# Optimization experiments

Hardware: AMD Instinct MI355X
Metric: run time of the kernel (lower is better)

The kernel has to match this reference:

```python
import jax, jax.numpy as jnp
import numpy as np

N_USERS = 50000
N_ITEMS = 50000
N_NODES = N_USERS + N_ITEMS
DIM = 64
NNZ = 3200000
N_LAYERS = 3


def setup_inputs() -> dict:
    key = jax.random.key(0)
    k1, k2, k3, k4, k5 = jax.random.split(key, 5)
    user_emb = 0.1 * jax.random.normal(k1, (N_USERS, DIM), dtype=jnp.float32)
    item_emb = 0.1 * jax.random.normal(k2, (N_ITEMS, DIM), dtype=jnp.float32)
    # COO representation of the symmetric normalized adjacency matrix
    adj_row = jax.random.randint(k3, (NNZ,), 0, N_NODES, dtype=jnp.int32)
    adj_col = jax.random.randint(k4, (NNZ,), 0, N_NODES, dtype=jnp.int32)
    # normalized adjacency values are small positive numbers (d_i^-1/2 d_j^-1/2)
    adj_vals = jax.random.uniform(k5, (NNZ,), dtype=jnp.float32) * 0.05
    return {"user_emb": user_emb, "item_emb": item_emb,
            "adj_vals": adj_vals, "adj_row": adj_row, "adj_col": adj_col}


def reference(user_emb, item_emb, adj_vals, adj_row, adj_col):
    # X0 = concat(user_embedding, item_embedding)  -> [N, D]
    x = jnp.concatenate([user_emb, item_emb], axis=0)

    def spmm(h):
        # sparse A @ h : gather source rows, scale by edge value, scatter-add to dest
        msgs = adj_vals[:, None] * h[adj_col]          # [nnz, D]
        return jax.ops.segment_sum(msgs, adj_row, num_segments=N_NODES)

    # three stacked LightGCN propagation layers (no transforms, no nonlinearity)
    for _ in range(N_LAYERS):
        x = spmm(x)
    return x
```

## Files before the change

kernel.cpp:

```cpp
#include <hip/hip_runtime.h>

#define DIM 64


#define SCAN_ELEMS 2048

typedef unsigned long long u64;


__global__ __launch_bounds__(256) void k_hist_slot(const int* __restrict__ rows,
                                                   int* __restrict__ counts,
                                                   int* __restrict__ slot, int nnz)
{
    for (int e = blockIdx.x * blockDim.x + threadIdx.x; e < nnz;
         e += gridDim.x * blockDim.x) {
        const int r = __builtin_nontemporal_load(rows + e);
        slot[e] = atomicAdd(counts + r, 1);
    }
}

__global__ __launch_bounds__(256) void k_hist(const int* __restrict__ rows,
                                              int* __restrict__ counts, int nnz)
{
    for (int e = blockIdx.x * blockDim.x + threadIdx.x; e < nnz;
         e += gridDim.x * blockDim.x)
        atomicAdd(counts + __builtin_nontemporal_load(rows + e), 1);
}

__global__ __launch_bounds__(256) void k_scan1(const int* __restrict__ counts,
                                               int* __restrict__ rp,
                                               int* __restrict__ blocksums, int n)
{
    __shared__ int lds[256];
    const int t = threadIdx.x, b = blockIdx.x;
    const int base = b * SCAN_ELEMS + t * 8;
    int v[8], s = 0;
#pragma unroll
    for (int k = 0; k < 8; ++k) {
        const int idx = base + k;
        v[k] = (idx < n) ? counts[idx] : 0;
        s += v[k];
    }
    lds[t] = s;
    __syncthreads();
    for (int off = 1; off < 256; off <<= 1) {
        const int val = (t >= off) ? lds[t - off] : 0;
        __syncthreads();
        lds[t] += val;
        __syncthreads();
    }
    const int incl = lds[t];
    if (t == 255) blocksums[b] = incl;
    int run = incl - s;
#pragma unroll
    for (int k = 0; k < 8; ++k) {
        const int idx = base + k;
        if (idx < n) rp[idx] = run;
        run += v[k];
    }
}

__global__ void k_scan2(int* __restrict__ blocksums, int nb)
{
    const int lane = threadIdx.x;
    const int v = (lane < nb) ? blocksums[lane] : 0;
    int incl = v;
    for (int off = 1; off < 64; off <<= 1) {
        const int t = __shfl_up(incl, off);
        if (lane >= off) incl += t;
    }
    if (lane < nb) blocksums[lane] = incl - v;
}

__global__ __launch_bounds__(256) void k_scan3(int* __restrict__ rp,
                                               const int* __restrict__ blocksums,
                                               int* __restrict__ cursor,
                                               int n, int nnz)
{
    for (int i = blockIdx.x * blockDim.x + threadIdx.x; i < n;
         i += gridDim.x * blockDim.x) {
        const int p = rp[i] + blocksums[i / SCAN_ELEMS];
        rp[i] = p;
        if (cursor) cursor[i] = p;
        if (i == 0) rp[n] = nnz;
    }
}

__global__ __launch_bounds__(256) void k_scatter_slot(
    const int* __restrict__ rows, const int* __restrict__ cols,
    const float* __restrict__ vals, const int* __restrict__ row_ptr,
    const int* __restrict__ slot, u64* __restrict__ edges, int nnz)
{
    for (int e = blockIdx.x * blockDim.x + threadIdx.x; e < nnz;
         e += gridDim.x * blockDim.x) {
        const int r = __builtin_nontemporal_load(rows + e);
        const int c = __builtin_nontemporal_load(cols + e);
        const float v = __builtin_nontemporal_load(vals + e);
        const int s = __builtin_nontemporal_load(slot + e);
        const u64 rec = ((u64)(unsigned)__float_as_int(v) << 32)
                      | (u64)(unsigned)c;
        edges[row_ptr[r] + s] = rec;
    }
}

__global__ __launch_bounds__(256) void k_scatter_cur(
    const int* __restrict__ rows, const int* __restrict__ cols,
    const float* __restrict__ vals, int* __restrict__ cursor,
    u64* __restrict__ edges, int nnz)
{
    for (int e = blockIdx.x * blockDim.x + threadIdx.x; e < nnz;
         e += gridDim.x * blockDim.x) {
        const int p = atomicAdd(cursor + __builtin_nontemporal_load(rows + e), 1);
        const u64 rec = ((u64)(unsigned)__float_as_int(
                             __builtin_nontemporal_load(vals + e)) << 32)
                      | (u64)(unsigned)__builtin_nontemporal_load(cols + e);
        edges[p] = rec;
    }
}


__global__ __launch_bounds__(256) void k_spmm(
    const float* __restrict__ x, const int* __restrict__ row_ptr,
    const u64* __restrict__ edges, float* __restrict__ y,
    int n, int rows_per_wave)
{
    const int lane = threadIdx.x & 63;
    const int w = (blockIdx.x * blockDim.x + threadIdx.x) >> 6;
    int r0 = w * rows_per_wave, r1 = r0 + rows_per_wave;
    if (r1 > n) r1 = n;
    for (int r = r0; r < r1; ++r) {
        const int start = __builtin_amdgcn_readfirstlane(row_ptr[r]);
        const int end   = __builtin_amdgcn_readfirstlane(row_ptr[r + 1]);
        float a0 = 0.f, a1 = 0.f, a2 = 0.f, a3 = 0.f;
        for (int j0 = start; j0 < end; j0 += 64) {
            const int nn = (end - j0 < 64) ? (end - j0) : 64;
            const u64 rec = __builtin_nontemporal_load(
                edges + j0 + ((lane < nn) ? lane : 0));
            const int lo = (int)(unsigned)(rec & 0xffffffffu);
            const int hi = (int)(unsigned)(rec >> 32);
            int k = 0;
            for (; k + 4 <= nn; k += 4) {
                const int   c0 = __builtin_amdgcn_readlane(lo, k + 0);
                const float v0 = __int_as_float(__builtin_amdgcn_readlane(hi, k + 0));
                const int   c1 = __builtin_amdgcn_readlane(lo, k + 1);
                const float v1 = __int_as_float(__builtin_amdgcn_readlane(hi, k + 1));
                const int   c2 = __builtin_amdgcn_readlane(lo, k + 2);
                const float v2 = __int_as_float(__builtin_amdgcn_readlane(hi, k + 2));
                const int   c3 = __builtin_amdgcn_readlane(lo, k + 3);
                const float v3 = __int_as_float(__builtin_amdgcn_readlane(hi, k + 3));
                a0 += v0 * x[(size_t)c0 * DIM + lane];
                a1 += v1 * x[(size_t)c1 * DIM + lane];
                a2 += v2 * x[(size_t)c2 * DIM + lane];
                a3 += v3 * x[(size_t)c3 * DIM + lane];
            }
            for (; k < nn; ++k) {
                const int   c = __builtin_amdgcn_readlane(lo, k);
                const float v = __int_as_float(__builtin_amdgcn_readlane(hi, k));
                a0 += v * x[(size_t)c * DIM + lane];
            }
        }
        y[(size_t)r * DIM + lane] = (a0 + a1) + (a2 + a3);
    }
}


__global__ __launch_bounds__(256) void lgcn_atomic(
    const float* __restrict__ x, const float* __restrict__ vals,
    const int* __restrict__ rows, const int* __restrict__ cols,
    float* __restrict__ y, int nnz, int edges_per_wave)
{
    const int lane = threadIdx.x & 63;
    const int wid = (blockIdx.x * blockDim.x + threadIdx.x) >> 6;
    int e0 = wid * edges_per_wave, e1 = e0 + edges_per_wave;
    if (e1 > nnz) e1 = nnz;
    for (int e = e0; e < e1; ++e) {
        const int eu = __builtin_amdgcn_readfirstlane(e);
        const float v = vals[eu];
        const float xv = x[(size_t)cols[eu] * DIM + lane];
        unsafeAtomicAdd(y + (size_t)rows[eu] * DIM + lane, v * xv);
    }
}


static inline size_t align256(size_t x) { return (x + 255) & ~(size_t)255; }

extern "C" void kernel_launch(void* const* d_in, const int* in_sizes, int n_in,
                              void* d_out, int out_size, void* d_ws, size_t ws_size,
                              hipStream_t stream)
{
    const float* user_emb = (const float*)d_in[0];
    const float* item_emb = (const float*)d_in[1];
    const float* vals     = (const float*)d_in[2];
    const int*   rows     = (const int*)d_in[3];
    const int*   cols     = (const int*)d_in[4];
    float*       out      = (float*)d_out;

    const int n   = (in_sizes[0] + in_sizes[1]) / DIM;
    const int nnz = in_sizes[2];

    const size_t u_bytes  = (size_t)in_sizes[0] * sizeof(float);
    const size_t i_bytes  = (size_t)in_sizes[1] * sizeof(float);
    const size_t x_bytes  = (size_t)n * DIM * sizeof(float);
    const size_t e_bytes  = (size_t)nnz * sizeof(u64);
    const size_t s_bytes  = (size_t)nnz * sizeof(int);
    const size_t rp_bytes = align256(((size_t)n + 1) * sizeof(int));

    size_t off = 0;
    float* x_mid  = (float*)((char*)d_ws + off); off += align256(x_bytes);
    u64*   edges  = (u64*)  ((char*)d_ws + off); off += align256(e_bytes);
    int*   row_ptr= (int*)  ((char*)d_ws + off); off += rp_bytes;
    int*   counts = (int*)  ((char*)d_ws + off); off += rp_bytes;
    int*   bsums  = (int*)  ((char*)d_ws + off); off += 256;
    const size_t need_cur = off;
    int*   slot   = (int*)  ((char*)d_ws + off); off += align256(s_bytes);
    const size_t need_full = off;
    int*   cursor = counts;

    const int blocks = 2048, threads = 256;
    const int nwaves = blocks * (threads / 64);

    hipMemcpyAsync(x_mid, user_emb, u_bytes, hipMemcpyDeviceToDevice, stream);
    hipMemcpyAsync((char*)x_mid + u_bytes, item_emb, i_bytes,
                   hipMemcpyDeviceToDevice, stream);

    if (ws_size >= need_cur) {
        const int nb = (n + SCAN_ELEMS - 1) / SCAN_ELEMS;
        const bool full = (ws_size >= need_full);
        hipMemsetAsync(counts, 0, (size_t)n * sizeof(int), stream);
        if (full)
            k_hist_slot<<<blocks, threads, 0, stream>>>(rows, counts, slot, nnz);
        else
            k_hist<<<blocks, threads, 0, stream>>>(rows, counts, nnz);
        k_scan1<<<nb, 256, 0, stream>>>(counts, row_ptr, bsums, n);
        k_scan2<<<1, 64, 0, stream>>>(bsums, nb);
        k_scan3<<<blocks, threads, 0, stream>>>(row_ptr, bsums,
                                                full ? (int*)nullptr : cursor,
                                                n, nnz);
        if (full)
            k_scatter_slot<<<blocks, threads, 0, stream>>>(rows, cols, vals,
                                                           row_ptr, slot, edges, nnz);
        else
            k_scatter_cur<<<blocks, threads, 0, stream>>>(rows, cols, vals,
                                                          cursor, edges, nnz);
        const int rpw = (n + nwaves - 1) / nwaves;
        k_spmm<<<blocks, threads, 0, stream>>>(x_mid, row_ptr, edges, out, n, rpw);
        k_spmm<<<blocks, threads, 0, stream>>>(out, row_ptr, edges, x_mid, n, rpw);
        k_spmm<<<blocks, threads, 0, stream>>>(x_mid, row_ptr, edges, out, n, rpw);
    } else {
        const int epw = (nnz + nwaves - 1) / nwaves;
        hipMemsetAsync(out, 0, x_bytes, stream);
        lgcn_atomic<<<blocks, threads, 0, stream>>>(x_mid, vals, rows, cols, out,
                                                    nnz, epw);
        hipMemsetAsync(x_mid, 0, x_bytes, stream);
        lgcn_atomic<<<blocks, threads, 0, stream>>>(out, vals, rows, cols, x_mid,
                                                    nnz, epw);
        hipMemsetAsync(out, 0, x_bytes, stream);
        lgcn_atomic<<<blocks, threads, 0, stream>>>(x_mid, vals, rows, cols, out,
                                                    nnz, epw);
    }
}
```

Measured before the change: 666.8 us.

## Build CSR with two-pass bucketed radix sort using LDS atomics

Replaces the global-atomic histogram and slot scatter used to build the CSR with a two-level bucketed counting sort. Rows are grouped into 1024-row buckets: per-block LDS histograms, a global scan over bucket-by-block counts, a scatter into bucket order, and then a per-bucket LDS histogram, scan and local scatter that writes row_ptr and the final edge array. This is meant to remove contended global atomics and the random 8-byte writes across the whole edge array. In exchange it adds an extra pass over a packed edge buffer, more workspace, and relies on column indices fitting in 17 bits.

```diff
diff --git a/kernel.cpp b/kernel.cpp
--- a/kernel.cpp
+++ b/kernel.cpp
@@ -4,28 +4,29 @@
 
 
 #define SCAN_ELEMS 2048
+#define NPB 1024
+#define BUCKET_SHIFT 10
 
 typedef unsigned long long u64;
 
 
-__global__ __launch_bounds__(256) void k_hist_slot(const int* __restrict__ rows,
-                                                   int* __restrict__ counts,
-                                                   int* __restrict__ slot, int nnz)
-{
-    for (int e = blockIdx.x * blockDim.x + threadIdx.x; e < nnz;
-         e += gridDim.x * blockDim.x) {
-        const int r = __builtin_nontemporal_load(rows + e);
-        slot[e] = atomicAdd(counts + r, 1);
-    }
-}
-
-__global__ __launch_bounds__(256) void k_hist(const int* __restrict__ rows,
-                                              int* __restrict__ counts, int nnz)
-{
-    for (int e = blockIdx.x * blockDim.x + threadIdx.x; e < nnz;
-         e += gridDim.x * blockDim.x)
-        atomicAdd(counts + __builtin_nontemporal_load(rows + e), 1);
-}
+__global__ __launch_bounds__(256) void k_pcount(const int* __restrict__ rows,
+                                                int* __restrict__ bcounts,
+                                                int nnz, int nb, int epb)
+{
+    __shared__ int h[128];
+    const int b = blockIdx.x;
+    for (int i = threadIdx.x; i < nb; i += 256) h[i] = 0;
+    __syncthreads();
+    const int e0 = b * epb;
+    const int e1 = (e0 + epb < nnz) ? e0 + epb : nnz;
+    for (int e = e0 + threadIdx.x; e < e1; e += 256)
+        atomicAdd(&h[__builtin_nontemporal_load(rows + e) >> BUCKET_SHIFT], 1);
+    __syncthreads();
+    for (int k = threadIdx.x; k < nb; k += 256)
+        bcounts[k * NPB + b] = h[k];
+}
+
 
 __global__ __launch_bounds__(256) void k_scan1(const int* __restrict__ counts,
                                                int* __restrict__ rp,
@@ -84,6 +85,98 @@
         if (cursor) cursor[i] = p;
         if (i == 0) rp[n] = nnz;
     }
+}
+
+
+__global__ __launch_bounds__(256) void k_pscatter(
+    const int* __restrict__ rows, const int* __restrict__ cols,
+    const float* __restrict__ vals, const int* __restrict__ scan_b,
+    u64* __restrict__ packed_p, int nnz, int nb, int epb)
+{
+    __shared__ int cur[128];
+    const int b = blockIdx.x;
+    for (int k = threadIdx.x; k < nb; k += 256) cur[k] = scan_b[k * NPB + b];
+    __syncthreads();
+    const int e0 = b * epb;
+    const int e1 = (e0 + epb < nnz) ? e0 + epb : nnz;
+    for (int e = e0 + threadIdx.x; e < e1; e += 256) {
+        const int r = __builtin_nontemporal_load(rows + e);
+        const int c = __builtin_nontemporal_load(cols + e);
+        const float v = __builtin_nontemporal_load(vals + e);
+        const int p = atomicAdd(&cur[r >> BUCKET_SHIFT], 1);
+        packed_p[p] = ((u64)(unsigned)__float_as_int(v) << 32)
+                    | ((u64)(unsigned)(r & 1023) << 17)
+                    | (u64)(unsigned)c;
+    }
+}
+
+
+__global__ __launch_bounds__(256) void k_bucket_csr(
+    const u64* __restrict__ packed_p, const int* __restrict__ scan_b,
+    int* __restrict__ row_ptr, u64* __restrict__ edges,
+    int n, int nnz, int nb)
+{
+    __shared__ int hist[1024];
+    __shared__ int wsum[256];
+    const int kb = blockIdx.x;
+    const int t = threadIdx.x;
+    const int bstart = scan_b[kb * NPB];
+    const int bend = (kb + 1 < nb) ? scan_b[(kb + 1) * NPB] : nnz;
+    for (int i = t; i < 1024; i += 256) hist[i] = 0;
+    __syncthreads();
+    for (int e = bstart + t; e < bend; e += 256)
+        atomicAdd(&hist[(int)((packed_p[e] >> 17) & 1023)], 1);
+    __syncthreads();
+    const int v0 = hist[4 * t + 0], v1 = hist[4 * t + 1];
+    const int v2 = hist[4 * t + 2], v3 = hist[4 * t + 3];
+    const int s = v0 + v1 + v2 + v3;
+    wsum[t] = s;
+    __syncthreads();
+    for (int off = 1; off < 256; off <<= 1) {
+        const int val = (t >= off) ? wsum[t - off] : 0;
+        __syncthreads();
+        wsum[t] += val;
+        __syncthreads();
+    }
+    const int run = wsum[t] - s;
+    hist[4 * t + 0] = run;
+    hist[4 * t + 1] = run + v0;
+    hist[4 * t + 2] = run + v0 + v1;
+    hist[4 * t + 3] = run + v0 + v1 + v2;
+    __syncthreads();
+    const int gbase = kb << BUCKET_SHIFT;
+    for (int i = t; i < 1024; i += 256) {
+        const int g = gbase + i;
+        if (g < n) row_ptr[g] = bstart + hist[i];
+    }
+    if (kb == 0 && t == 0) row_ptr[n] = nnz;
+    __syncthreads();
+    for (int e = bstart + t; e < bend; e += 256) {
+        const u64 rec = packed_p[e];
+        const int r = (int)((rec >> 17) & 1023);
+        const int p = bstart + atomicAdd(&hist[r], 1);
+        edges[p] = (rec & 0xFFFFFFFF00000000ULL) | (rec & 0x1FFFFULL);
+    }
+}
+
+
+__global__ __launch_bounds__(256) void k_hist_slot(const int* __restrict__ rows,
+                                                   int* __restrict__ counts,
+                                                   int* __restrict__ slot, int nnz)
+{
+    for (int e = blockIdx.x * blockDim.x + threadIdx.x; e < nnz;
+         e += gridDim.x * blockDim.x) {
+        const int r = __builtin_nontemporal_load(rows + e);
+        slot[e] = atomicAdd(counts + r, 1);
+    }
+}
+
+__global__ __launch_bounds__(256) void k_hist(const int* __restrict__ rows,
+                                              int* __restrict__ counts, int nnz)
+{
+    for (int e = blockIdx.x * blockDim.x + threadIdx.x; e < nnz;
+         e += gridDim.x * blockDim.x)
+        atomicAdd(counts + __builtin_nontemporal_load(rows + e), 1);
 }
 
 __global__ __launch_bounds__(256) void k_scatter_slot(
@@ -202,37 +295,66 @@
     const size_t i_bytes  = (size_t)in_sizes[1] * sizeof(float);
     const size_t x_bytes  = (size_t)n * DIM * sizeof(float);
     const size_t e_bytes  = (size_t)nnz * sizeof(u64);
-    const size_t s_bytes  = (size_t)nnz * sizeof(int);
     const size_t rp_bytes = align256(((size_t)n + 1) * sizeof(int));
+
+    const int nb  = (n + (1 << BUCKET_SHIFT) - 1) >> BUCKET_SHIFT;
+    const int n2  = nb * NPB;
+    const int epb = (nnz + NPB - 1) / NPB;
+    const size_t b_bytes = align256(((size_t)n2 + 256) * sizeof(int));
+
+    const int blocks = 2048, threads = 256;
+    const int nwaves = blocks * (threads / 64);
 
     size_t off = 0;
     float* x_mid  = (float*)((char*)d_ws + off); off += align256(x_bytes);
     u64*   edges  = (u64*)  ((char*)d_ws + off); off += align256(e_bytes);
     int*   row_ptr= (int*)  ((char*)d_ws + off); off += rp_bytes;
-    int*   counts = (int*)  ((char*)d_ws + off); off += rp_bytes;
-    int*   bsums  = (int*)  ((char*)d_ws + off); off += 256;
-    const size_t need_cur = off;
-    int*   slot   = (int*)  ((char*)d_ws + off); off += align256(s_bytes);
-    const size_t need_full = off;
+
+    size_t roff = off;
+    int*   bcounts = (int*)((char*)d_ws + roff); roff += b_bytes;
+    int*   scan_b  = (int*)((char*)d_ws + roff); roff += b_bytes;
+    int*   bsums_r = (int*)((char*)d_ws + roff); roff += 256;
+    u64*   packed_p= (u64*)((char*)d_ws + roff); roff += align256(e_bytes);
+    const size_t need_radix = roff;
+
+    size_t hoff = off;
+    int*   counts = (int*)((char*)d_ws + hoff); hoff += rp_bytes;
+    int*   bsums  = (int*)((char*)d_ws + hoff); hoff += 256;
+    const size_t need_cur = hoff;
+    int*   slot   = (int*)((char*)d_ws + hoff); hoff += align256((size_t)nnz * sizeof(int));
+    const size_t need_full = hoff;
     int*   cursor = counts;
-
-    const int blocks = 2048, threads = 256;
-    const int nwaves = blocks * (threads / 64);
 
     hipMemcpyAsync(x_mid, user_emb, u_bytes, hipMemcpyDeviceToDevice, stream);
     hipMemcpyAsync((char*)x_mid + u_bytes, item_emb, i_bytes,
                    hipMemcpyDeviceToDevice, stream);
 
-    if (ws_size >= need_cur) {
-        const int nb = (n + SCAN_ELEMS - 1) / SCAN_ELEMS;
+    const int rpw = (n + nwaves - 1) / nwaves;
+
+    if (ws_size >= need_radix) {
+        const int nb2 = (n2 + SCAN_ELEMS - 1) / SCAN_ELEMS;
+        k_pcount<<<NPB, threads, 0, stream>>>(rows, bcounts, nnz, nb, epb);
+        k_scan1<<<nb2, 256, 0, stream>>>(bcounts, scan_b, bsums_r, n2);
+        k_scan2<<<1, 64, 0, stream>>>(bsums_r, nb2);
+        k_scan3<<<blocks, threads, 0, stream>>>(scan_b, bsums_r, (int*)nullptr,
+                                                n2, nnz);
+        k_pscatter<<<NPB, threads, 0, stream>>>(rows, cols, vals, scan_b,
+                                                packed_p, nnz, nb, epb);
+        k_bucket_csr<<<nb, threads, 0, stream>>>(packed_p, scan_b, row_ptr,
+                                                 edges, n, nnz, nb);
+        k_spmm<<<blocks, threads, 0, stream>>>(x_mid, row_ptr, edges, out, n, rpw);
+        k_spmm<<<blocks, threads, 0, stream>>>(out, row_ptr, edges, x_mid, n, rpw);
+        k_spmm<<<blocks, threads, 0, stream>>>(x_mid, row_ptr, edges, out, n, rpw);
+    } else if (ws_size >= need_cur) {
+        const int nbs = (n + SCAN_ELEMS - 1) / SCAN_ELEMS;
         const bool full = (ws_size >= need_full);
         hipMemsetAsync(counts, 0, (size_t)n * sizeof(int), stream);
         if (full)
             k_hist_slot<<<blocks, threads, 0, stream>>>(rows, counts, slot, nnz);
         else
             k_hist<<<blocks, threads, 0, stream>>>(rows, counts, nnz);
-        k_scan1<<<nb, 256, 0, stream>>>(counts, row_ptr, bsums, n);
-        k_scan2<<<1, 64, 0, stream>>>(bsums, nb);
+        k_scan1<<<nbs, 256, 0, stream>>>(counts, row_ptr, bsums, n);
+        k_scan2<<<1, 64, 0, stream>>>(bsums, nbs);
         k_scan3<<<blocks, threads, 0, stream>>>(row_ptr, bsums,
                                                 full ? (int*)nullptr : cursor,
                                                 n, nnz);
@@ -242,7 +364,6 @@
         else
             k_scatter_cur<<<blocks, threads, 0, stream>>>(rows, cols, vals,
                                                           cursor, edges, nnz);
-        const int rpw = (n + nwaves - 1) / nwaves;
         k_spmm<<<blocks, threads, 0, stream>>>(x_mid, row_ptr, edges, out, n, rpw);
         k_spmm<<<blocks, threads, 0, stream>>>(out, row_ptr, edges, x_mid, n, rpw);
         k_spmm<<<blocks, threads, 0, stream>>>(x_mid, row_ptr, edges, out, n, rpw);
```

New measurement: 570.4 us. 1.17x faster.
